# Performance work log

Measured on AMD Instinct MI355X. Metric: run time of the kernel, lower is better.

Reference implementation:

```python
import jax, jax.numpy as jnp
import numpy as np

N = 100000   # nodes
E = 1250000  # directed edges
F = 32       # node_features
H = 64       # hidden_channels
C = 10       # num_classes
NEG_SLOPE = 0.2  # GATConv default LeakyReLU slope


def _glorot(key, shape):
    fan_in = shape[0]
    return jax.random.normal(key, shape, jnp.float32) / np.sqrt(fan_in)


def setup_inputs() -> dict:
    k = jax.random.split(jax.random.key(0), 16)
    x = jax.random.normal(k[0], (N, F), jnp.float32)
    edge_index = jax.random.randint(k[1], (2, E), 0, N, dtype=jnp.int32)
    return {
        "x": x,
        "edge_index": edge_index,
        # GCNConv 1
        "W1": _glorot(k[2], (F, H)), "b1": jnp.zeros((H,), jnp.float32),
        # GATConv (heads=1)
        "W2": _glorot(k[3], (H, H)),
        "a_src": _glorot(k[4], (H,)), "a_dst": _glorot(k[5], (H,)),
        "b2": jnp.zeros((H,), jnp.float32),
        # GCNConv 3
        "W3": _glorot(k[6], (H, H)), "b3": jnp.zeros((H,), jnp.float32),
        # optimization head
        "Wopt": _glorot(k[7], (H, C)), "bopt": jnp.zeros((C,), jnp.float32),
        # bottleneck detector MLP
        "Wb1": _glorot(k[8], (H, 32)), "bb1": jnp.zeros((32,), jnp.float32),
        "Wb2": _glorot(k[9], (32, 1)), "bb2": jnp.zeros((1,), jnp.float32),
    }


def _gcn_conv(x, W, b, src, dst, n):
    # PyG GCNConv: self-loops already appended to src/dst by caller.
    h = x @ W  # [n, out]
    deg = jnp.zeros((n,), x.dtype).at[dst].add(1.0)
    dinv = jax.lax.rsqrt(jnp.maximum(deg, 1e-12))
    norm = dinv[src] * dinv[dst]  # [e]
    msg = h[src] * norm[:, None]  # gather + scale
    out = jnp.zeros_like(h).at[dst].add(msg)  # scatter-add
    return out + b


def _gat_conv(x, W, a_src, a_dst, b, src, dst, n):
    # PyG GATConv, heads=1: self-loops already appended.
    h = x @ W  # [n, out]
    alpha_s = h @ a_src  # [n]
    alpha_d = h @ a_dst  # [n]
    e = jax.nn.leaky_relu(alpha_s[src] + alpha_d[dst], NEG_SLOPE)  # [e]
    # softmax over incoming edges of each dst node
    emax = jax.ops.segment_max(e, dst, num_segments=n)
    p = jnp.exp(e - emax[dst])
    denom = jax.ops.segment_sum(p, dst, num_segments=n)
    alpha = p / denom[dst]
    out = jnp.zeros_like(h).at[dst].add(h[src] * alpha[:, None])
    return out + b


def reference(x, edge_index, W1, b1, W2, a_src, a_dst, b2, W3, b3,
              Wopt, bopt, Wb1, bb1, Wb2, bb2):
    n = x.shape[0]
    loops = jnp.arange(n, dtype=edge_index.dtype)
    src = jnp.concatenate([edge_index[0], loops])
    dst = jnp.concatenate([edge_index[1], loops])

    h = jax.nn.relu(_gcn_conv(x, W1, b1, src, dst, n))
    h = jax.nn.relu(_gat_conv(h, W2, a_src, a_dst, b2, src, dst, n))
    h = jax.nn.relu(_gcn_conv(h, W3, b3, src, dst, n))

    optimizations = h @ Wopt + bopt                     # [n, C]
    bottlenecks = jax.nn.sigmoid(jax.nn.relu(h @ Wb1 + bb1) @ Wb2 + bb2)  # [n, 1]
    graph_embedding = h.mean(axis=0)                    # [H]
    return optimizations, bottlenecks, graph_embedding
```

## Files before the change

### kernel.cpp

```cpp
#include <hip/hip_runtime.h>
#include <hip/hip_bf16.h>


#define CAP 64
#define NSLICE 4

__device__ __forceinline__ int uwave(){
  return __builtin_amdgcn_readfirstlane(threadIdx.x >> 6);
}
__device__ __forceinline__ unsigned short f2bf(float f){
  unsigned u = __float_as_uint(f);
  return (unsigned short)((u + 0x7fffu + ((u >> 16) & 1u)) >> 16);
}
__device__ __forceinline__ float bfl(unsigned u){ return __uint_as_float(u << 16); }
__device__ __forceinline__ float bfh(unsigned u){ return __uint_as_float(u & 0xffff0000u); }

__global__ void k_setup(const float* __restrict__ Wopt, const float* __restrict__ bopt,
                        const float* __restrict__ Wb1, const float* __restrict__ bb1,
                        float* __restrict__ Wcat, float* __restrict__ bcat,
                        int* __restrict__ cnt, unsigned short* __restrict__ tb,
                        unsigned short* __restrict__ xh, float* __restrict__ emb_acc,
                        int n){
  int i = blockIdx.x*blockDim.x + threadIdx.x;
  if (i < n) cnt[i] = 0;
  if (blockIdx.x == 0){
    int tid = threadIdx.x;
    for (int j = tid; j < 4096; j += 256){
      int f = j >> 6, c = j & 63;
      float w = 0.f;
      if (c < 10)       w = Wopt[f*10 + c];
      else if (c >= 32) w = Wb1[f*32 + (c-32)];
      Wcat[j] = w;
    }
    if (tid < 64){
      float b = 0.f;
      if (tid < 10)       b = bopt[tid];
      else if (tid >= 32) b = bb1[tid-32];
      bcat[tid] = b;
      tb[(size_t)n*64 + tid] = 0;
      emb_acc[tid] = 0.f;
    }
    if (tid >= 64 && tid < 96) xh[(size_t)n*32 + (tid-64)] = 0;
  }
}

__global__ void k_hist(const int* __restrict__ src, const int* __restrict__ dst,
                       int* __restrict__ cnt, int* __restrict__ adj,
                       int e, int nper){
  int slice = blockIdx.x & (NSLICE-1);
  int i = (blockIdx.x / NSLICE)*blockDim.x + threadIdx.x;
  if (i >= e) return;
  int d = __builtin_nontemporal_load(&dst[i]);
  int lo = slice*nper;
  if (d < lo || d >= lo + nper) return;
  int pos = atomicAdd(&cnt[d], 1);
  if (pos < CAP){
    int sv = __builtin_nontemporal_load(&src[i]);
    adj[(size_t)d*CAP + pos] = sv;
  }
}

__global__ void k_castscale(const float* __restrict__ x, const int* __restrict__ cnt,
                            unsigned short* __restrict__ xh, int total4){
  int i = blockIdx.x*blockDim.x + threadIdx.x;
  if (i >= total4) return;
  int row = i >> 3;
  float dv = rsqrtf((float)(cnt[row] + 1));
  float4 v = ((const float4*)x)[i];
  uint2 o;
  o.x = (unsigned)f2bf(v.x*dv) | ((unsigned)f2bf(v.y*dv) << 16);
  o.y = (unsigned)f2bf(v.z*dv) | ((unsigned)f2bf(v.w*dv) << 16);
  ((uint2*)xh)[i] = o;
}

__global__ __launch_bounds__(256) void k_agg32g(const unsigned short* __restrict__ xh,
                          const int* __restrict__ adj, const int* __restrict__ cnt,
                          const float* __restrict__ W1, const float* __restrict__ b1,
                          unsigned short* __restrict__ h, int n){
  int lane = threadIdx.x & 63;
  float wreg[32];
  #pragma unroll
  for (int k = 0; k < 32; k++) wreg[k] = W1[k*64 + lane];
  float br = b1[lane];
  int v0 = blockIdx.x*8 + uwave()*2;
  if (v0 >= n) return;
  int v1 = v0 + 1;
  bool has1 = v1 < n;
  if (!has1) v1 = v0;
  int cn0 = cnt[v0], cn1 = cnt[v1];
  int c0 = min(cn0, CAP), c1 = min(cn1, CAP);
  int ureg0 = n, ureg1 = n;
  if (lane < c0) ureg0 = (adj + (size_t)v0*CAP)[lane];
  if (lane < c1) ureg1 = (adj + (size_t)v1*CAP)[lane];
  int g = lane >> 3, q = lane & 7;
  float4 a0 = {0.f,0.f,0.f,0.f}, a1 = {0.f,0.f,0.f,0.f};
  int itm = (max(c0, c1) + 7) >> 3;
  #pragma unroll 2
  for (int jj = 0; jj < itm; jj++){
    int u0 = __shfl(ureg0, jj*8 + g);
    int u1 = __shfl(ureg1, jj*8 + g);
    uint2 r0 = ((const uint2*)(xh + (size_t)u0*32))[q];
    uint2 r1 = ((const uint2*)(xh + (size_t)u1*32))[q];
    a0.x += bfl(r0.x); a0.y += bfh(r0.x); a0.z += bfl(r0.y); a0.w += bfh(r0.y);
    a1.x += bfl(r1.x); a1.y += bfh(r1.x); a1.z += bfl(r1.y); a1.w += bfh(r1.y);
  }
  #pragma unroll
  for (int off = 8; off <= 32; off <<= 1){
    a0.x += __shfl_xor(a0.x, off); a0.y += __shfl_xor(a0.y, off);
    a0.z += __shfl_xor(a0.z, off); a0.w += __shfl_xor(a0.w, off);
    a1.x += __shfl_xor(a1.x, off); a1.y += __shfl_xor(a1.y, off);
    a1.z += __shfl_xor(a1.z, off); a1.w += __shfl_xor(a1.w, off);
  }
  uint2 s0 = ((const uint2*)(xh + (size_t)v0*32))[q];
  uint2 s1 = ((const uint2*)(xh + (size_t)v1*32))[q];
  a0.x += bfl(s0.x); a0.y += bfh(s0.x); a0.z += bfl(s0.y); a0.w += bfh(s0.y);
  a1.x += bfl(s1.x); a1.y += bfh(s1.x); a1.z += bfl(s1.y); a1.w += bfh(s1.y);
  float dv0 = rsqrtf((float)(cn0 + 1)), dv1 = rsqrtf((float)(cn1 + 1));
  a0.x *= dv0; a0.y *= dv0; a0.z *= dv0; a0.w *= dv0;
  a1.x *= dv1; a1.y *= dv1; a1.z *= dv1; a1.w *= dv1;
  float h0 = br, h1v = br;
  #pragma unroll
  for (int q2 = 0; q2 < 8; q2++){
    float4 w0, w1;
    w0.x = __shfl(a0.x, q2); w0.y = __shfl(a0.y, q2);
    w0.z = __shfl(a0.z, q2); w0.w = __shfl(a0.w, q2);
    w1.x = __shfl(a1.x, q2); w1.y = __shfl(a1.y, q2);
    w1.z = __shfl(a1.z, q2); w1.w = __shfl(a1.w, q2);
    h0 = fmaf(w0.x, wreg[q2*4+0], h0); h1v = fmaf(w1.x, wreg[q2*4+0], h1v);
    h0 = fmaf(w0.y, wreg[q2*4+1], h0); h1v = fmaf(w1.y, wreg[q2*4+1], h1v);
    h0 = fmaf(w0.z, wreg[q2*4+2], h0); h1v = fmaf(w1.z, wreg[q2*4+2], h1v);
    h0 = fmaf(w0.w, wreg[q2*4+3], h0); h1v = fmaf(w1.w, wreg[q2*4+3], h1v);
  }
  h[(size_t)v0*64 + lane] = f2bf(fmaxf(h0, 0.f));
  if (has1) h[(size_t)v1*64 + lane] = f2bf(fmaxf(h1v, 0.f));
}

template<bool SCALE>
__global__ __launch_bounds__(256, 4) void k_gemm_b(const unsigned short* __restrict__ x,
                       const float* __restrict__ W, const int* __restrict__ cnt,
                       unsigned short* __restrict__ t, int n){
  int lane = threadIdx.x & 63;
  int gw = blockIdx.x*4 + uwave();
  int nw = gridDim.x*4;
  float wreg[64];
  #pragma unroll
  for (int k = 0; k < 64; k++) wreg[k] = W[k*64 + lane];
  for (int v = gw; v < n; v += nw){
    const uint4* xr = (const uint4*)(x + (size_t)v*64);
    float acc = 0.f;
    #pragma unroll
    for (int k8 = 0; k8 < 8; k8++){
      uint4 c = xr[k8];
      acc = fmaf(bfl(c.x), wreg[k8*8+0], acc);
      acc = fmaf(bfh(c.x), wreg[k8*8+1], acc);
      acc = fmaf(bfl(c.y), wreg[k8*8+2], acc);
      acc = fmaf(bfh(c.y), wreg[k8*8+3], acc);
      acc = fmaf(bfl(c.z), wreg[k8*8+4], acc);
      acc = fmaf(bfh(c.z), wreg[k8*8+5], acc);
      acc = fmaf(bfl(c.w), wreg[k8*8+6], acc);
      acc = fmaf(bfh(c.w), wreg[k8*8+7], acc);
    }
    if (SCALE) acc *= rsqrtf((float)(cnt[v] + 1));
    t[(size_t)v*64 + lane] = f2bf(acc);
  }
}

__global__ __launch_bounds__(256, 4) void k_gemm_alpha(const unsigned short* __restrict__ x,
                       const float* __restrict__ W,
                       const float* __restrict__ asrc, const float* __restrict__ adst,
                       unsigned short* __restrict__ t, float* __restrict__ als,
                       float* __restrict__ ald, int n){
  int lane = threadIdx.x & 63;
  int gw = blockIdx.x*4 + uwave();
  int nw = gridDim.x*4;
  float wreg[64];
  #pragma unroll
  for (int k = 0; k < 64; k++) wreg[k] = W[k*64 + lane];
  float asr = asrc[lane], adr = adst[lane];
  for (int v = gw; v < n; v += nw){
    const uint4* xr = (const uint4*)(x + (size_t)v*64);
    float acc = 0.f;
    #pragma unroll
    for (int k8 = 0; k8 < 8; k8++){
      uint4 c = xr[k8];
      acc = fmaf(bfl(c.x), wreg[k8*8+0], acc);
      acc = fmaf(bfh(c.x), wreg[k8*8+1], acc);
      acc = fmaf(bfl(c.y), wreg[k8*8+2], acc);
      acc = fmaf(bfh(c.y), wreg[k8*8+3], acc);
      acc = fmaf(bfl(c.z), wreg[k8*8+4], acc);
      acc = fmaf(bfh(c.z), wreg[k8*8+5], acc);
      acc = fmaf(bfl(c.w), wreg[k8*8+6], acc);
      acc = fmaf(bfh(c.w), wreg[k8*8+7], acc);
    }
    t[(size_t)v*64 + lane] = f2bf(acc);
    float s1 = acc * asr, s2 = acc * adr;
    #pragma unroll
    for (int off = 32; off; off >>= 1){
      s1 += __shfl_xor(s1, off);
      s2 += __shfl_xor(s2, off);
    }
    if (lane == 0){ als[v] = s1; ald[v] = s2; }
  }
}

__global__ __launch_bounds__(256) void k_gcn_agg(const unsigned short* __restrict__ t,
                          const int* __restrict__ adj, const int* __restrict__ cnt,
                          const float* __restrict__ b, unsigned short* __restrict__ h, int n){
  int lane = threadIdx.x & 63;
  int v0 = blockIdx.x*8 + uwave()*2;
  if (v0 >= n) return;
  int v1 = v0 + 1;
  bool has1 = v1 < n;
  if (!has1) v1 = v0;
  int cn0 = cnt[v0], cn1 = cnt[v1];
  int c0 = min(cn0, CAP), c1 = min(cn1, CAP);
  int ureg0 = n, ureg1 = n;
  if (lane < c0) ureg0 = (adj + (size_t)v0*CAP)[lane];
  if (lane < c1) ureg1 = (adj + (size_t)v1*CAP)[lane];
  int g = lane >> 3, q = lane & 7;
  float a0[8] = {0,0,0,0,0,0,0,0}, a1[8] = {0,0,0,0,0,0,0,0};
  int itm = (max(c0, c1) + 7) >> 3;
  #pragma unroll 2
  for (int jj = 0; jj < itm; jj++){
    int u0 = __shfl(ureg0, jj*8 + g);
    int u1 = __shfl(ureg1, jj*8 + g);
    uint4 r0 = ((const uint4*)(t + (size_t)u0*64))[q];
    uint4 r1 = ((const uint4*)(t + (size_t)u1*64))[q];
    a0[0] += bfl(r0.x); a0[1] += bfh(r0.x); a0[2] += bfl(r0.y); a0[3] += bfh(r0.y);
    a0[4] += bfl(r0.z); a0[5] += bfh(r0.z); a0[6] += bfl(r0.w); a0[7] += bfh(r0.w);
    a1[0] += bfl(r1.x); a1[1] += bfh(r1.x); a1[2] += bfl(r1.y); a1[3] += bfh(r1.y);
    a1[4] += bfl(r1.z); a1[5] += bfh(r1.z); a1[6] += bfl(r1.w); a1[7] += bfh(r1.w);
  }
  #pragma unroll
  for (int off = 8; off <= 32; off <<= 1){
    #pragma unroll
    for (int k = 0; k < 8; k++){
      a0[k] += __shfl_xor(a0[k], off);
      a1[k] += __shfl_xor(a1[k], off);
    }
  }
  uint4 s0 = ((const uint4*)(t + (size_t)v0*64))[q];
  uint4 s1 = ((const uint4*)(t + (size_t)v1*64))[q];
  a0[0] += bfl(s0.x); a0[1] += bfh(s0.x); a0[2] += bfl(s0.y); a0[3] += bfh(s0.y);
  a0[4] += bfl(s0.z); a0[5] += bfh(s0.z); a0[6] += bfl(s0.w); a0[7] += bfh(s0.w);
  a1[0] += bfl(s1.x); a1[1] += bfh(s1.x); a1[2] += bfl(s1.y); a1[3] += bfh(s1.y);
  a1[4] += bfl(s1.z); a1[5] += bfh(s1.z); a1[6] += bfl(s1.w); a1[7] += bfh(s1.w);
  float dv0 = rsqrtf((float)(cn0 + 1)), dv1 = rsqrtf((float)(cn1 + 1));
  float4 b0 = ((const float4*)b)[2*q], b1v = ((const float4*)b)[2*q+1];
  if (g == 0){
    float r0 = fmaxf(fmaf(a0[0], dv0, b0.x), 0.f),  r1 = fmaxf(fmaf(a0[1], dv0, b0.y), 0.f);
    float r2 = fmaxf(fmaf(a0[2], dv0, b0.z), 0.f),  r3 = fmaxf(fmaf(a0[3], dv0, b0.w), 0.f);
    float r4 = fmaxf(fmaf(a0[4], dv0, b1v.x), 0.f), r5 = fmaxf(fmaf(a0[5], dv0, b1v.y), 0.f);
    float r6 = fmaxf(fmaf(a0[6], dv0, b1v.z), 0.f), r7 = fmaxf(fmaf(a0[7], dv0, b1v.w), 0.f);
    uint4 o;
    o.x = (unsigned)f2bf(r0) | ((unsigned)f2bf(r1) << 16);
    o.y = (unsigned)f2bf(r2) | ((unsigned)f2bf(r3) << 16);
    o.z = (unsigned)f2bf(r4) | ((unsigned)f2bf(r5) << 16);
    o.w = (unsigned)f2bf(r6) | ((unsigned)f2bf(r7) << 16);
    ((uint4*)(h + (size_t)v0*64))[q] = o;
  } else if (g == 1 && has1){
    float r0 = fmaxf(fmaf(a1[0], dv1, b0.x), 0.f),  r1 = fmaxf(fmaf(a1[1], dv1, b0.y), 0.f);
    float r2 = fmaxf(fmaf(a1[2], dv1, b0.z), 0.f),  r3 = fmaxf(fmaf(a1[3], dv1, b0.w), 0.f);
    float r4 = fmaxf(fmaf(a1[4], dv1, b1v.x), 0.f), r5 = fmaxf(fmaf(a1[5], dv1, b1v.y), 0.f);
    float r6 = fmaxf(fmaf(a1[6], dv1, b1v.z), 0.f), r7 = fmaxf(fmaf(a1[7], dv1, b1v.w), 0.f);
    uint4 o;
    o.x = (unsigned)f2bf(r0) | ((unsigned)f2bf(r1) << 16);
    o.y = (unsigned)f2bf(r2) | ((unsigned)f2bf(r3) << 16);
    o.z = (unsigned)f2bf(r4) | ((unsigned)f2bf(r5) << 16);
    o.w = (unsigned)f2bf(r6) | ((unsigned)f2bf(r7) << 16);
    ((uint4*)(h + (size_t)v1*64))[q] = o;
  }
}

__global__ __launch_bounds__(256) void k_gat_agg(const unsigned short* __restrict__ t,
                          const int* __restrict__ adj, const int* __restrict__ cnt,
                          const float* __restrict__ als, const float* __restrict__ ald,
                          const float* __restrict__ b, unsigned short* __restrict__ h, int n){
  int lane = threadIdx.x & 63;
  int v0 = blockIdx.x*8 + uwave()*2;
  if (v0 >= n) return;
  int v1 = v0 + 1;
  bool has1 = v1 < n;
  if (!has1) v1 = v0;
  int c0 = min(cnt[v0], CAP), c1 = min(cnt[v1], CAP);
  int ureg0 = n, ureg1 = n;
  if (lane < c0) ureg0 = (adj + (size_t)v0*CAP)[lane];
  if (lane < c1) ureg1 = (adj + (size_t)v1*CAP)[lane];
  int us0 = (lane < c0) ? ureg0 : v0;
  int us1 = (lane < c1) ? ureg1 : v1;
  float adv0 = ald[v0], adv1 = ald[v1];
  float e0 = als[us0] + adv0;
  float e1 = als[us1] + adv1;
  e0 = e0 > 0.f ? e0 : 0.2f*e0;
  e1 = e1 > 0.f ? e1 : 0.2f*e1;
  float es0 = als[v0] + adv0; es0 = es0 > 0.f ? es0 : 0.2f*es0;
  float es1 = als[v1] + adv1; es1 = es1 > 0.f ? es1 : 0.2f*es1;
  float em0 = (lane < c0) ? e0 : -1e30f;
  float em1 = (lane < c1) ? e1 : -1e30f;
  #pragma unroll
  for (int off = 32; off; off >>= 1){
    em0 = fmaxf(em0, __shfl_xor(em0, off));
    em1 = fmaxf(em1, __shfl_xor(em1, off));
  }
  em0 = fmaxf(em0, es0); em1 = fmaxf(em1, es1);
  float p0 = (lane < c0) ? __expf(e0 - em0) : 0.f;
  float p1 = (lane < c1) ? __expf(e1 - em1) : 0.f;
  float sm0 = p0, sm1 = p1;
  #pragma unroll
  for (int off = 32; off; off >>= 1){
    sm0 += __shfl_xor(sm0, off);
    sm1 += __shfl_xor(sm1, off);
  }
  float ps0 = __expf(es0 - em0), ps1 = __expf(es1 - em1);
  float inv0 = 1.f / (sm0 + ps0), inv1 = 1.f / (sm1 + ps1);
  int g = lane >> 3, q = lane & 7;
  float a0[8] = {0,0,0,0,0,0,0,0}, a1[8] = {0,0,0,0,0,0,0,0};
  int itm = (max(c0, c1) + 7) >> 3;
  #pragma unroll 2
  for (int jj = 0; jj < itm; jj++){
    int   u0 = __shfl(ureg0, jj*8 + g);
    int   u1 = __shfl(ureg1, jj*8 + g);
    float w0 = __shfl(p0,    jj*8 + g);
    float w1 = __shfl(p1,    jj*8 + g);
    uint4 r0 = ((const uint4*)(t + (size_t)u0*64))[q];
    uint4 r1 = ((const uint4*)(t + (size_t)u1*64))[q];
    a0[0] = fmaf(w0, bfl(r0.x), a0[0]); a0[1] = fmaf(w0, bfh(r0.x), a0[1]);
    a0[2] = fmaf(w0, bfl(r0.y), a0[2]); a0[3] = fmaf(w0, bfh(r0.y), a0[3]);
    a0[4] = fmaf(w0, bfl(r0.z), a0[4]); a0[5] = fmaf(w0, bfh(r0.z), a0[5]);
    a0[6] = fmaf(w0, bfl(r0.w), a0[6]); a0[7] = fmaf(w0, bfh(r0.w), a0[7]);
    a1[0] = fmaf(w1, bfl(r1.x), a1[0]); a1[1] = fmaf(w1, bfh(r1.x), a1[1]);
    a1[2] = fmaf(w1, bfl(r1.y), a1[2]); a1[3] = fmaf(w1, bfh(r1.y), a1[3]);
    a1[4] = fmaf(w1, bfl(r1.z), a1[4]); a1[5] = fmaf(w1, bfh(r1.z), a1[5]);
    a1[6] = fmaf(w1, bfl(r1.w), a1[6]); a1[7] = fmaf(w1, bfh(r1.w), a1[7]);
  }
  #pragma unroll
  for (int off = 8; off <= 32; off <<= 1){
    #pragma unroll
    for (int k = 0; k < 8; k++){
      a0[k] += __shfl_xor(a0[k], off);
      a1[k] += __shfl_xor(a1[k], off);
    }
  }
  uint4 s0 = ((const uint4*)(t + (size_t)v0*64))[q];
  uint4 s1 = ((const uint4*)(t + (size_t)v1*64))[q];
  a0[0] = fmaf(ps0, bfl(s0.x), a0[0]); a0[1] = fmaf(ps0, bfh(s0.x), a0[1]);
  a0[2] = fmaf(ps0, bfl(s0.y), a0[2]); a0[3] = fmaf(ps0, bfh(s0.y), a0[3]);
  a0[4] = fmaf(ps0, bfl(s0.z), a0[4]); a0[5] = fmaf(ps0, bfh(s0.z), a0[5]);
  a0[6] = fmaf(ps0, bfl(s0.w), a0[6]); a0[7] = fmaf(ps0, bfh(s0.w), a0[7]);
  a1[0] = fmaf(ps1, bfl(s1.x), a1[0]); a1[1] = fmaf(ps1, bfh(s1.x), a1[1]);
  a1[2] = fmaf(ps1, bfl(s1.y), a1[2]); a1[3] = fmaf(ps1, bfh(s1.y), a1[3]);
  a1[4] = fmaf(ps1, bfl(s1.z), a1[4]); a1[5] = fmaf(ps1, bfh(s1.z), a1[5]);
  a1[6] = fmaf(ps1, bfl(s1.w), a1[6]); a1[7] = fmaf(ps1, bfh(s1.w), a1[7]);
  float4 b0 = ((const float4*)b)[2*q], b1v = ((const float4*)b)[2*q+1];
  if (g == 0){
    float r0 = fmaxf(fmaf(a0[0], inv0, b0.x), 0.f),  r1 = fmaxf(fmaf(a0[1], inv0, b0.y), 0.f);
    float r2 = fmaxf(fmaf(a0[2], inv0, b0.z), 0.f),  r3 = fmaxf(fmaf(a0[3], inv0, b0.w), 0.f);
    float r4 = fmaxf(fmaf(a0[4], inv0, b1v.x), 0.f), r5 = fmaxf(fmaf(a0[5], inv0, b1v.y), 0.f);
    float r6 = fmaxf(fmaf(a0[6], inv0, b1v.z), 0.f), r7 = fmaxf(fmaf(a0[7], inv0, b1v.w), 0.f);
    uint4 o;
    o.x = (unsigned)f2bf(r0) | ((unsigned)f2bf(r1) << 16);
    o.y = (unsigned)f2bf(r2) | ((unsigned)f2bf(r3) << 16);
    o.z = (unsigned)f2bf(r4) | ((unsigned)f2bf(r5) << 16);
    o.w = (unsigned)f2bf(r6) | ((unsigned)f2bf(r7) << 16);
    ((uint4*)(h + (size_t)v0*64))[q] = o;
  } else if (g == 1 && has1){
    float r0 = fmaxf(fmaf(a1[0], inv1, b0.x), 0.f),  r1 = fmaxf(fmaf(a1[1], inv1, b0.y), 0.f);
    float r2 = fmaxf(fmaf(a1[2], inv1, b0.z), 0.f),  r3 = fmaxf(fmaf(a1[3], inv1, b0.w), 0.f);
    float r4 = fmaxf(fmaf(a1[4], inv1, b1v.x), 0.f), r5 = fmaxf(fmaf(a1[5], inv1, b1v.y), 0.f);
    float r6 = fmaxf(fmaf(a1[6], inv1, b1v.z), 0.f), r7 = fmaxf(fmaf(a1[7], inv1, b1v.w), 0.f);
    uint4 o;
    o.x = (unsigned)f2bf(r0) | ((unsigned)f2bf(r1) << 16);
    o.y = (unsigned)f2bf(r2) | ((unsigned)f2bf(r3) << 16);
    o.z = (unsigned)f2bf(r4) | ((unsigned)f2bf(r5) << 16);
    o.w = (unsigned)f2bf(r6) | ((unsigned)f2bf(r7) << 16);
    ((uint4*)(h + (size_t)v1*64))[q] = o;
  }
}

__global__ __launch_bounds__(256, 4) void k_heads(const unsigned short* __restrict__ h,
                        const float* __restrict__ Wcat, const float* __restrict__ bcat,
                        const float* __restrict__ Wb2, const float* __restrict__ bb2,
                        float* __restrict__ out_opt, float* __restrict__ out_bot, int n){
  int lane = threadIdx.x & 63;
  int gw = blockIdx.x*4 + uwave();
  int nw = gridDim.x*4;
  float wreg[64];
  #pragma unroll
  for (int k = 0; k < 64; k++) wreg[k] = Wcat[k*64 + lane];
  float bcr  = bcat[lane];
  float wb2r = (lane >= 32) ? Wb2[lane-32] : 0.f;
  float bb2r = bb2[0];
  for (int v = gw; v < n; v += nw){
    const uint4* xr = (const uint4*)(h + (size_t)v*64);
    float acc = bcr;
    #pragma unroll
    for (int k8 = 0; k8 < 8; k8++){
      uint4 c = xr[k8];
      acc = fmaf(bfl(c.x), wreg[k8*8+0], acc);
      acc = fmaf(bfh(c.x), wreg[k8*8+1], acc);
      acc = fmaf(bfl(c.y), wreg[k8*8+2], acc);
      acc = fmaf(bfh(c.y), wreg[k8*8+3], acc);
      acc = fmaf(bfl(c.z), wreg[k8*8+4], acc);
      acc = fmaf(bfh(c.z), wreg[k8*8+5], acc);
      acc = fmaf(bfl(c.w), wreg[k8*8+6], acc);
      acc = fmaf(bfh(c.w), wreg[k8*8+7], acc);
    }
    if (lane < 10) out_opt[(size_t)v*10 + lane] = acc;
    float contrib = fmaxf(acc, 0.f) * wb2r;
    #pragma unroll
    for (int off = 32; off; off >>= 1) contrib += __shfl_xor(contrib, off);
    if (lane == 0) out_bot[v] = 1.f / (1.f + __expf(-(contrib + bb2r)));
  }
}

__global__ __launch_bounds__(256) void k_mean(const unsigned short* __restrict__ h,
                       float* __restrict__ emb_acc, int n){
  __shared__ float red[256];
  int tid = threadIdx.x;
  int w = tid >> 6, lane = tid & 63;
  float s = 0.f;
  for (int r = blockIdx.x*4 + w; r < n; r += 1024)
    s += __uint_as_float(((unsigned)h[(size_t)r*64 + lane]) << 16);
  red[tid] = s;
  __syncthreads();
  if (tid < 64)
    atomicAdd(&emb_acc[tid], red[tid] + red[64+tid] + red[128+tid] + red[192+tid]);
}

__global__ void k_embed(const float* __restrict__ emb_acc, float* __restrict__ out_emb,
                        float invn){
  if (threadIdx.x < 64) out_emb[threadIdx.x] = emb_acc[threadIdx.x] * invn;
}

extern "C" void kernel_launch(void* const* d_in, const int* in_sizes, int n_in,
                              void* d_out, int out_size, void* d_ws, size_t ws_size,
                              hipStream_t stream) {
  const float* x    = (const float*)d_in[0];
  const int*   ei   = (const int*)d_in[1];
  const float* W1   = (const float*)d_in[2];
  const float* b1   = (const float*)d_in[3];
  const float* W2   = (const float*)d_in[4];
  const float* a_s  = (const float*)d_in[5];
  const float* a_d  = (const float*)d_in[6];
  const float* b2   = (const float*)d_in[7];
  const float* W3   = (const float*)d_in[8];
  const float* b3   = (const float*)d_in[9];
  const float* Wopt = (const float*)d_in[10];
  const float* bopt = (const float*)d_in[11];
  const float* Wb1  = (const float*)d_in[12];
  const float* bb1  = (const float*)d_in[13];
  const float* Wb2  = (const float*)d_in[14];
  const float* bb2  = (const float*)d_in[15];

  int n = in_sizes[0] / 32;
  int e = in_sizes[1] / 2;
  const int* src = ei;
  const int* dst = ei + e;

  char* ws = (char*)d_ws;
  size_t off = 0;
  auto alloc = [&](size_t bytes) -> void* {
    void* p = ws + off;
    off += (bytes + 255) & ~(size_t)255;
    return p;
  };
  int*            cnt     = (int*)           alloc((size_t)n * 4);
  int*            adj     = (int*)           alloc((size_t)n * CAP * 4);
  float*          als     = (float*)         alloc((size_t)n * 4);
  float*          ald     = (float*)         alloc((size_t)n * 4);
  unsigned short* xh      = (unsigned short*)alloc((size_t)(n+1) * 32 * 2);
  unsigned short* tb      = (unsigned short*)alloc((size_t)(n+1) * 64 * 2);
  unsigned short* hbuf    = (unsigned short*)alloc((size_t)n * 64 * 2);
  float*          emb_acc = (float*)         alloc((size_t)64 * 4);
  float*          Wcat    = (float*)         alloc((size_t)4096 * 4);
  float*          bcat    = (float*)         alloc((size_t)64 * 4);

  float* out_opt = (float*)d_out;
  float* out_bot = out_opt + (size_t)n * 10;
  float* out_emb = out_bot + n;

  int nb8    = (n + 7) / 8;
  int nbN    = (n + 255) / 256;
  int nbE    = (e + 255) / 256;
  int nper   = (n + NSLICE - 1) / NSLICE;
  int total4 = n*32/4;
  int nbC    = (total4 + 255) / 256;

  k_setup<<<nbN, 256, 0, stream>>>(Wopt, bopt, Wb1, bb1, Wcat, bcat,
                                   cnt, tb, xh, emb_acc, n);
  k_hist<<<nbE*NSLICE, 256, 0, stream>>>(src, dst, cnt, adj, e, nper);
  k_castscale<<<nbC, 256, 0, stream>>>(x, cnt, xh, total4);

  k_agg32g<<<nb8, 256, 0, stream>>>(xh, adj, cnt, W1, b1, hbuf, n);

  k_gemm_alpha<<<1024, 256, 0, stream>>>(hbuf, W2, a_s, a_d, tb, als, ald, n);
  k_gat_agg<<<nb8, 256, 0, stream>>>(tb, adj, cnt, als, ald, b2, hbuf, n);

  k_gemm_b<true><<<1024, 256, 0, stream>>>(hbuf, W3, cnt, tb, n);
  k_gcn_agg<<<nb8, 256, 0, stream>>>(tb, adj, cnt, b3, hbuf, n);

  k_heads<<<1024, 256, 0, stream>>>(hbuf, Wcat, bcat, Wb2, bb2,
                                    out_opt, out_bot, n);
  k_mean<<<256, 256, 0, stream>>>(hbuf, emb_acc, n);
  k_embed<<<1, 64, 0, stream>>>(emb_acc, out_emb, 1.0f / (float)n);
}
```

Baseline: 398.9 us.

## Replace sliced edge histogram with bucket partition then per-bucket adjacency fill

Drops the four-pass sliced edge scan, which reread the dst array once per destination slice. Edges are now partitioned once into 8 destination-range buckets of (dst, src) pairs, using shared-memory counters and one global atomic per block per bucket. A second kernel walks each bucket and fills the capped adjacency lists, so the atomics and scattered writes for a bucket land in a narrower address range that should stay cache-resident. The pair staging buffer borrows the hbuf workspace, and pairs beyond the fixed per-bucket capacity are silently dropped.

```diff
diff --git a/kernel.cpp b/kernel.cpp
--- a/kernel.cpp
+++ b/kernel.cpp
@@ -3,7 +3,9 @@
 
 
 #define CAP 64
-#define NSLICE 4
+#define NBUK 8
+
+typedef unsigned uvec4 __attribute__((ext_vector_type(4)));
 
 __device__ __forceinline__ int uwave(){
   return __builtin_amdgcn_readfirstlane(threadIdx.x >> 6);
@@ -18,7 +20,8 @@
 __global__ void k_setup(const float* __restrict__ Wopt, const float* __restrict__ bopt,
                         const float* __restrict__ Wb1, const float* __restrict__ bb1,
                         float* __restrict__ Wcat, float* __restrict__ bcat,
-                        int* __restrict__ cnt, unsigned short* __restrict__ tb,
+                        int* __restrict__ cnt, int* __restrict__ bcnt,
+                        unsigned short* __restrict__ tb,
                         unsigned short* __restrict__ xh, float* __restrict__ emb_acc,
                         int n){
   int i = blockIdx.x*blockDim.x + threadIdx.x;
@@ -41,22 +44,69 @@
       emb_acc[tid] = 0.f;
     }
     if (tid >= 64 && tid < 96) xh[(size_t)n*32 + (tid-64)] = 0;
-  }
-}
-
-__global__ void k_hist(const int* __restrict__ src, const int* __restrict__ dst,
-                       int* __restrict__ cnt, int* __restrict__ adj,
-                       int e, int nper){
-  int slice = blockIdx.x & (NSLICE-1);
-  int i = (blockIdx.x / NSLICE)*blockDim.x + threadIdx.x;
-  if (i >= e) return;
-  int d = __builtin_nontemporal_load(&dst[i]);
-  int lo = slice*nper;
-  if (d < lo || d >= lo + nper) return;
-  int pos = atomicAdd(&cnt[d], 1);
-  if (pos < CAP){
-    int sv = __builtin_nontemporal_load(&src[i]);
-    adj[(size_t)d*CAP + pos] = sv;
+    if (tid >= 96 && tid < 96 + NBUK) bcnt[tid-96] = 0;
+  }
+}
+
+__global__ __launch_bounds__(256) void k_part(const int* __restrict__ src,
+                        const int* __restrict__ dst,
+                        uint2* __restrict__ pairs, int* __restrict__ bcnt,
+                        int e, int pbcap, float binv){
+  __shared__ int lcnt[NBUK];
+  __shared__ int lbase[NBUK];
+  int tid = threadIdx.x;
+  if (tid < NBUK) lcnt[tid] = 0;
+  __syncthreads();
+  int i0 = blockIdx.x*1024 + tid*4;
+  int d[4], s[4], bk[4], lp[4];
+  int nv = e - i0;
+  if (nv > 4) nv = 4;
+  if (nv == 4){
+    int4 dd = *(const int4*)(dst + i0);
+    int4 ss = *(const int4*)(src + i0);
+    d[0]=dd.x; d[1]=dd.y; d[2]=dd.z; d[3]=dd.w;
+    s[0]=ss.x; s[1]=ss.y; s[2]=ss.z; s[3]=ss.w;
+  } else {
+    #pragma unroll
+    for (int j = 0; j < 4; j++){ d[j] = 0; s[j] = 0; }
+    for (int j = 0; j < nv; j++){ d[j] = dst[i0+j]; s[j] = src[i0+j]; }
+  }
+  #pragma unroll
+  for (int j = 0; j < 4; j++){
+    if (j < nv){
+      bk[j] = min(NBUK-1, (int)((float)d[j] * binv));
+      lp[j] = atomicAdd(&lcnt[bk[j]], 1);
+    }
+  }
+  __syncthreads();
+  if (tid < NBUK) lbase[tid] = atomicAdd(&bcnt[tid], lcnt[tid]);
+  __syncthreads();
+  #pragma unroll
+  for (int j = 0; j < 4; j++){
+    if (j < nv){
+      int p = lbase[bk[j]] + lp[j];
+      if (p < pbcap)
+        pairs[(size_t)bk[j]*pbcap + p] = make_uint2((unsigned)d[j], (unsigned)s[j]);
+    }
+  }
+}
+
+__global__ __launch_bounds__(256) void k_fill(const uint2* __restrict__ pairs,
+                        const int* __restrict__ bcnt, int* __restrict__ cnt,
+                        int* __restrict__ adj, int pbcap){
+  int b = blockIdx.x & (NBUK-1);
+  int m = bcnt[b];
+  if (m > pbcap) m = pbcap;
+  const uvec4* pb = (const uvec4*)(pairs + (size_t)b*pbcap);
+  int half = (m + 1) >> 1;
+  int tpb = (gridDim.x >> 3) * 256;
+  for (int j = (blockIdx.x >> 3)*256 + threadIdx.x; j < half; j += tpb){
+    uvec4 p = __builtin_nontemporal_load(pb + j);
+    int pos0 = atomicAdd(&cnt[p.x], 1);
+    bool ok1 = (2*j + 1) < m;
+    int pos1 = ok1 ? atomicAdd(&cnt[p.z], 1) : 0;
+    if (pos0 < CAP) adj[(size_t)p.x*CAP + pos0] = (int)p.y;
+    if (ok1 && pos1 < CAP) adj[(size_t)p.z*CAP + pos1] = (int)p.w;
   }
 }
 
@@ -474,6 +524,10 @@
   float*          emb_acc = (float*)         alloc((size_t)64 * 4);
   float*          Wcat    = (float*)         alloc((size_t)4096 * 4);
   float*          bcat    = (float*)         alloc((size_t)64 * 4);
+  int*            bcnt    = (int*)           alloc((size_t)NBUK * 4);
+
+  int pbcap = e / NBUK + 8192;
+  uint2* pairs = (uint2*)hbuf;
 
   float* out_opt = (float*)d_out;
   float* out_bot = out_opt + (size_t)n * 10;
@@ -481,14 +535,14 @@
 
   int nb8    = (n + 7) / 8;
   int nbN    = (n + 255) / 256;
-  int nbE    = (e + 255) / 256;
-  int nper   = (n + NSLICE - 1) / NSLICE;
+  int nbP    = (e + 1023) / 1024;
   int total4 = n*32/4;
   int nbC    = (total4 + 255) / 256;
 
   k_setup<<<nbN, 256, 0, stream>>>(Wopt, bopt, Wb1, bb1, Wcat, bcat,
-                                   cnt, tb, xh, emb_acc, n);
-  k_hist<<<nbE*NSLICE, 256, 0, stream>>>(src, dst, cnt, adj, e, nper);
+                                   cnt, bcnt, tb, xh, emb_acc, n);
+  k_part<<<nbP, 256, 0, stream>>>(src, dst, pairs, bcnt, e, pbcap, 8.0f/(float)n);
+  k_fill<<<2048, 256, 0, stream>>>(pairs, bcnt, cnt, adj, pbcap);
   k_castscale<<<nbC, 256, 0, stream>>>(x, cnt, xh, total4);
 
   k_agg32g<<<nb8, 256, 0, stream>>>(xh, adj, cnt, W1, b1, hbuf, n);
```

After: 413.2 us. 1.04x slower.
